# Optimization experiments

Measured on AMD Instinct MI355X. Metric: run time of the kernel, lower is better.

Reference implementation:

```python
import jax, jax.numpy as jnp
import numpy as np

B, N, C, H = 8, 1024, 1024, 16
HD = C // H
SCALE = HD ** -0.5


def setup_inputs() -> dict:
    key = jax.random.key(0)
    ks = jax.random.split(key, 6)
    s = 0.02
    return {
        "x": jax.random.normal(ks[0], (B, N, C), dtype=jnp.float32),
        "z_cls": jax.random.normal(ks[1], (B, 2 * C), dtype=jnp.float32),
        "Wqkv": jax.random.normal(ks[2], (C, 3 * C), dtype=jnp.float32) * s,
        "Wkv_cls": jax.random.normal(ks[3], (2 * C, 2 * C), dtype=jnp.float32) * s,
        "Wproj": jax.random.normal(ks[4], (C, C), dtype=jnp.float32) * s,
        "bproj": jax.random.normal(ks[5], (C,), dtype=jnp.float32) * s,
    }


def reference(x, z_cls, Wqkv, Wkv_cls, Wproj, bproj):
    # qkv projection: [B,N,3C] -> q,k,v each [B,H,N,HD]
    qkv = (x @ Wqkv).reshape(B, N, 3, H, HD).transpose(2, 0, 3, 1, 4)
    q, k, v = qkv[0], qkv[1], qkv[2]
    # cls k/v: [B,2C] -> [B,H,1,HD] each
    kv_cls = (z_cls @ Wkv_cls).reshape(B, 1, 2, H, HD).transpose(2, 0, 3, 1, 4)
    k_cls, v_cls = kv_cls[0], kv_cls[1]
    k = jnp.concatenate([k_cls, k], axis=2)  # [B,H,N+1,HD]
    v = jnp.concatenate([v_cls, v], axis=2)
    attn = jax.nn.softmax(jnp.einsum("bhnd,bhmd->bhnm", q, k) * SCALE, axis=-1)
    out = jnp.einsum("bhnm,bhmd->bhnd", attn, v)  # [B,H,N,HD]
    out = out.transpose(0, 2, 1, 3).reshape(B, N, C)
    return out @ Wproj + bproj
```

## Files before the change

### kernel.cpp

```cpp
#include <hip/hip_runtime.h>


typedef __attribute__((ext_vector_type(8))) short bf16x8;
typedef __attribute__((ext_vector_type(8))) unsigned short u16x8;
typedef __attribute__((ext_vector_type(4))) float f32x4;

#define SL2E 0.18033688011112042f

__device__ __forceinline__ unsigned short f2bf(float f) {
  unsigned int u = __builtin_bit_cast(unsigned int, f);
  return (unsigned short)((u + 0x7FFFu + ((u >> 16) & 1u)) >> 16);
}

__device__ __forceinline__ unsigned int cvt_pk_bf16(float lo, float hi) {
  unsigned int r;
  asm("v_cvt_pk_bf16_f32 %0, %1, %2" : "=v"(r) : "v"(lo), "v"(hi));
  return r;
}

template <typename T>
__device__ __forceinline__ void gll16(const T* g, void* l) {
  __builtin_amdgcn_global_load_lds(
      (__attribute__((address_space(1))) void*)(const_cast<T*>(g)),
      (__attribute__((address_space(3))) void*)l, 16, 0, 0);
}

__global__ __launch_bounds__(256) void cvt_f2b(const float* __restrict__ in,
                                               unsigned short* __restrict__ out, int n) {
  int i = (blockIdx.x * 256 + threadIdx.x) * 8;
  if (i >= n) return;
  const float4* p4 = (const float4*)(in + i);
  float4 a = p4[0], b = p4[1];
  u16x8 o;
  o[0] = f2bf(a.x); o[1] = f2bf(a.y); o[2] = f2bf(a.z); o[3] = f2bf(a.w);
  o[4] = f2bf(b.x); o[5] = f2bf(b.y); o[6] = f2bf(b.z); o[7] = f2bf(b.w);
  *(u16x8*)(out + i) = o;
}

__global__ __launch_bounds__(256) void transpose_f2b(const float* __restrict__ in,
                                                     unsigned short* __restrict__ out,
                                                     int R, int C) {
  __shared__ float tile[32][33];
  int c0 = blockIdx.x * 32, r0 = blockIdx.y * 32;
  int tx = threadIdx.x, ty = threadIdx.y;
#pragma unroll
  for (int j = 0; j < 32; j += 8)
    tile[ty + j][tx] = in[(size_t)(r0 + ty + j) * C + c0 + tx];
  __syncthreads();
#pragma unroll
  for (int j = 0; j < 32; j += 8)
    out[(size_t)(c0 + ty + j) * R + r0 + tx] = f2bf(tile[tx][ty + j]);
}

__global__ __launch_bounds__(256) void kvcls_gemm(const float* __restrict__ z,
                                                  const float* __restrict__ W,
                                                  float* __restrict__ accum) {
  int cc = blockIdx.x >> 5;
  int kc = blockIdx.x & 31;
  int c = cc * 256 + threadIdx.x;
  int k0 = kc * 64;
  float acc[8] = {0, 0, 0, 0, 0, 0, 0, 0};
  const float* wp = W + (size_t)k0 * 2048 + c;
  for (int k = 0; k < 64; ++k) {
    float wv = wp[(size_t)k * 2048];
#pragma unroll
    for (int b = 0; b < 8; ++b) acc[b] += z[b * 2048 + k0 + k] * wv;
  }
#pragma unroll
  for (int b = 0; b < 8; ++b) atomicAdd(&accum[b * 2048 + c], acc[b]);
}

__global__ __launch_bounds__(256) void kvcls_scatter(const float* __restrict__ accum,
                                                     unsigned short* __restrict__ kbuf,
                                                     unsigned short* __restrict__ vbuf) {
  int i = blockIdx.x * 256 + threadIdx.x;
  int b = i >> 11, c = i & 2047;
  int t = c >> 10, h = (c >> 6) & 15, d = c & 63;
  int bh = b * 16 + h;
  unsigned short v = f2bf(accum[i]);
  if (t == 0) kbuf[((size_t)bh * 1088 + 0) * 64 + d] = v;
  else        vbuf[((size_t)bh * 64 + d) * 1088 + 0] = v;
}

__global__ __launch_bounds__(512, 2) void gemm_qkv(const unsigned short* __restrict__ A,
                                                   const unsigned short* __restrict__ Bt,
                                                   unsigned short* __restrict__ qb,
                                                   unsigned short* __restrict__ kbuf,
                                                   unsigned short* __restrict__ vbuf) {
  __shared__ __attribute__((aligned(16))) unsigned short As[2][256 * 64];
  __shared__ __attribute__((aligned(16))) unsigned short Bs[2][256 * 64];
  int t = threadIdx.x, w = t >> 6, l = t & 63;
  int g = l >> 4, q = l & 15;
  int wg = ((int)blockIdx.x & 7) * 48 + ((int)blockIdx.x >> 3);
  int tm = wg / 12, tn = wg % 12;
  int m0 = tm * 256, n0 = tn * 256;
  int wr = w >> 2, wc = w & 3;

  auto STAGE = [&](int bb, int k0) {
#pragma unroll
    for (int i = 0; i < 4; ++i) {
      int f = i * 8192 + t * 16;
      int row = f >> 7, colb = (f & 127) ^ ((row & 7) << 4);
      gll16(A + (size_t)(m0 + row) * 1024 + k0 + (colb >> 1), (char*)As[bb] + f);
    }
#pragma unroll
    for (int i = 0; i < 4; ++i) {
      int f = i * 8192 + t * 16;
      int row = f >> 7, colb = (f & 127) ^ ((row & 7) << 4);
      gll16(Bt + (size_t)(n0 + row) * 1024 + k0 + (colb >> 1), (char*)Bs[bb] + f);
    }
  };

  f32x4 acc[8][4] = {};
  STAGE(0, 0);
  for (int kt = 0; kt < 16; ++kt) {
    int cur = kt & 1;
    if (kt < 15) {
      STAGE(cur ^ 1, (kt + 1) * 64);
      asm volatile("s_waitcnt vmcnt(8)" ::: "memory");
    } else {
      asm volatile("s_waitcnt vmcnt(0)" ::: "memory");
    }
    __builtin_amdgcn_s_barrier();
    asm volatile("" ::: "memory");
    const char* Ac = (const char*)As[cur];
    const char* Bc = (const char*)Bs[cur];
#pragma unroll
    for (int kk = 0; kk < 2; ++kk) {
      bf16x8 af[8], bf[4];
#pragma unroll
      for (int m = 0; m < 8; ++m) {
        int row = wr * 128 + m * 16 + q;
        af[m] = *(const bf16x8*)(Ac + row * 128 + ((kk * 64 + g * 16) ^ ((row & 7) << 4)));
      }
#pragma unroll
      for (int n = 0; n < 4; ++n) {
        int row = wc * 64 + n * 16 + q;
        bf[n] = *(const bf16x8*)(Bc + row * 128 + ((kk * 64 + g * 16) ^ ((row & 7) << 4)));
      }
      __builtin_amdgcn_s_setprio(1);
#pragma unroll
      for (int m = 0; m < 8; ++m)
#pragma unroll
        for (int n = 0; n < 4; ++n)
          acc[m][n] = __builtin_amdgcn_mfma_f32_16x16x32_bf16(af[m], bf[n], acc[m][n], 0, 0, 0);
      __builtin_amdgcn_s_setprio(0);
    }
    asm volatile("" ::: "memory");
    __builtin_amdgcn_s_barrier();
    asm volatile("" ::: "memory");
  }
  int tsel = n0 >> 10;
  int b = m0 >> 10;
  int nqb = m0 & 1023, ncb = n0 & 1023;
#pragma unroll
  for (int m = 0; m < 8; ++m)
#pragma unroll
    for (int n = 0; n < 4; ++n)
#pragma unroll
      for (int r = 0; r < 4; ++r) {
        int nq = nqb + wr * 128 + m * 16 + g * 4 + r;
        int col = ncb + wc * 64 + n * 16 + q;
        int h = col >> 6, d = col & 63;
        int bh = b * 16 + h;
        unsigned short val = f2bf(acc[m][n][r]);
        if (tsel == 0)      qb[((size_t)bh * 1024 + nq) * 64 + d] = val;
        else if (tsel == 1) kbuf[((size_t)bh * 1088 + 1 + nq) * 64 + d] = val;
        else                vbuf[((size_t)bh * 64 + d) * 1088 + 1 + nq] = val;
      }
}

__global__ __launch_bounds__(256) void attn_kernel(const unsigned short* __restrict__ qbuf,
                                                   const unsigned short* __restrict__ kbuf,
                                                   const unsigned short* __restrict__ vbuf,
                                                   unsigned short* __restrict__ ob) {
  __shared__ __attribute__((aligned(16))) unsigned short Ks[2][64 * 64];
  __shared__ __attribute__((aligned(16))) unsigned short Vs[2][64 * 64];
  __shared__ __attribute__((aligned(16))) unsigned short Ps[4][16 * 64];
  int t = threadIdx.x, w = t >> 6, l = t & 63;
  int g = l >> 4, q = l & 15;
  int wg = (blockIdx.x & 7) * 256 + (blockIdx.x >> 3);
  int bh = wg >> 4, qt = wg & 15;

  const unsigned short* qrow = qbuf + ((size_t)bh * 1024 + qt * 64 + w * 16 + q) * 64;
  bf16x8 qf[2];
  qf[0] = *(const bf16x8*)(qrow + g * 8);
  qf[1] = *(const bf16x8*)(qrow + 32 + g * 8);

  const unsigned short* kg = kbuf + (size_t)bh * 1088 * 64;
  const unsigned short* vg = vbuf + (size_t)bh * 64 * 1088;
  char* Pw = (char*)Ps[w];

  auto STAGE = [&](int bb, int kt) {
#pragma unroll
    for (int i = 0; i < 2; ++i) {
      int f = i * 4096 + t * 16;
      int row = f >> 7, colb = (f & 127) ^ ((row & 7) << 4);
      gll16(kg + (size_t)(kt * 64 + row) * 64 + (colb >> 1), (char*)Ks[bb] + f);
      gll16(vg + (size_t)row * 1088 + kt * 64 + (colb >> 1), (char*)Vs[bb] + f);
    }
  };

  STAGE(0, 0);
  __syncthreads();

  f32x4 o[4] = {};
  float mrun = -__builtin_inff(), lrun = 0.f;
  int swz = (q & 7) << 4;

  for (int kt = 0; kt < 17; ++kt) {
    int cur = kt & 1;
    if (kt < 16) STAGE(cur ^ 1, kt + 1);
    f32x4 s[4] = {};
#pragma unroll
    for (int kk = 0; kk < 2; ++kk) {
      bf16x8 kf[4];
#pragma unroll
      for (int n = 0; n < 4; ++n) {
        int cb = (kk * 64 + g * 16) ^ swz;
        kf[n] = *(const bf16x8*)((const char*)Ks[cur] + (n * 16 + q) * 128 + cb);
      }
      __builtin_amdgcn_s_setprio(1);
#pragma unroll
      for (int n = 0; n < 4; ++n)
        s[n] = __builtin_amdgcn_mfma_f32_16x16x32_bf16(kf[n], qf[kk], s[n], 0, 0, 0);
      __builtin_amdgcn_s_setprio(0);
    }
    if (kt == 16) {
#pragma unroll
      for (int n = 0; n < 4; ++n)
#pragma unroll
        for (int r = 0; r < 4; ++r)
          if (n | r) s[n][r] = -__builtin_inff();
      if (g != 0) s[0][0] = -__builtin_inff();
    }
    float mx = fmaxf(fmaxf(fmaxf(s[0][0], s[0][1]), fmaxf(s[0][2], s[0][3])),
                     fmaxf(fmaxf(s[1][0], s[1][1]), fmaxf(s[1][2], s[1][3])));
    mx = fmaxf(mx, fmaxf(fmaxf(fmaxf(s[2][0], s[2][1]), fmaxf(s[2][2], s[2][3])),
                         fmaxf(fmaxf(s[3][0], s[3][1]), fmaxf(s[3][2], s[3][3]))));
    mx = fmaxf(mx, __shfl_xor(mx, 16));
    mx = fmaxf(mx, __shfl_xor(mx, 32));
    float mnew;
    if (__all(mx <= mrun + 64.f)) {
      mnew = mrun;
    } else {
      mnew = fmaxf(mrun, mx);
      float fc = exp2f((mrun - mnew) * SL2E);
      mrun = mnew;
      lrun *= fc;
#pragma unroll
      for (int n = 0; n < 4; ++n) {
        o[n][0] *= fc; o[n][1] *= fc; o[n][2] *= fc; o[n][3] *= fc;
      }
    }
    float nb = mnew * SL2E;
    float rs = 0.f;
#pragma unroll
    for (int n = 0; n < 4; ++n)
#pragma unroll
      for (int r = 0; r < 4; ++r) {
        float p = exp2f(s[n][r] * SL2E - nb);
        s[n][r] = p;
        rs += p;
      }
    rs += __shfl_xor(rs, 16);
    rs += __shfl_xor(rs, 32);
    lrun += rs;
#pragma unroll
    for (int n = 0; n < 4; ++n) {
      uint2 pk;
      pk.x = cvt_pk_bf16(s[n][0], s[n][1]);
      pk.y = cvt_pk_bf16(s[n][2], s[n][3]);
      *(uint2*)(Pw + q * 128 + ((n * 32 + g * 8) ^ swz)) = pk;
    }
    asm volatile("s_waitcnt lgkmcnt(0)" ::: "memory");
#pragma unroll
    for (int kk = 0; kk < 2; ++kk) {
      bf16x8 pb = *(const bf16x8*)(Pw + q * 128 + ((kk * 64 + g * 16) ^ swz));
      bf16x8 vf[4];
#pragma unroll
      for (int n = 0; n < 4; ++n) {
        int cb = (kk * 64 + g * 16) ^ swz;
        vf[n] = *(const bf16x8*)((const char*)Vs[cur] + (n * 16 + q) * 128 + cb);
      }
      __builtin_amdgcn_s_setprio(1);
#pragma unroll
      for (int n = 0; n < 4; ++n)
        o[n] = __builtin_amdgcn_mfma_f32_16x16x32_bf16(vf[n], pb, o[n], 0, 0, 0);
      __builtin_amdgcn_s_setprio(0);
    }
    __syncthreads();
  }
  int b = bh >> 4, h = bh & 15;
  float inv = 1.0f / lrun;
  size_t rowg = (size_t)b * 1024 + qt * 64 + w * 16 + q;
#pragma unroll
  for (int n = 0; n < 4; ++n) {
    uint2 pk;
    pk.x = cvt_pk_bf16(o[n][0] * inv, o[n][1] * inv);
    pk.y = cvt_pk_bf16(o[n][2] * inv, o[n][3] * inv);
    *(uint2*)(ob + rowg * 1024 + h * 64 + n * 16 + g * 4) = pk;
  }
}

__global__ __launch_bounds__(512, 2) void gemm_proj(const unsigned short* __restrict__ A,
                                                    const unsigned short* __restrict__ Bt,
                                                    const float* __restrict__ bias,
                                                    float* __restrict__ out) {
  __shared__ __attribute__((aligned(16))) unsigned short As[2][256 * 64];
  __shared__ __attribute__((aligned(16))) unsigned short Bs[2][128 * 64];
  int t = threadIdx.x, w = t >> 6, l = t & 63;
  int g = l >> 4, q = l & 15;
  int wg = ((int)blockIdx.x & 7) * 32 + ((int)blockIdx.x >> 3);
  int tm = wg / 8, tn = wg % 8;
  int m0 = tm * 256, n0 = tn * 128;
  int wr = w >> 2, wc = w & 3;

  auto STAGE = [&](int bb, int k0) {
#pragma unroll
    for (int i = 0; i < 4; ++i) {
      int f = i * 8192 + t * 16;
      int row = f >> 7, colb = (f & 127) ^ ((row & 7) << 4);
      gll16(A + (size_t)(m0 + row) * 1024 + k0 + (colb >> 1), (char*)As[bb] + f);
    }
#pragma unroll
    for (int i = 0; i < 2; ++i) {
      int f = i * 8192 + t * 16;
      int row = f >> 7, colb = (f & 127) ^ ((row & 7) << 4);
      gll16(Bt + (size_t)(n0 + row) * 1024 + k0 + (colb >> 1), (char*)Bs[bb] + f);
    }
  };

  f32x4 acc[8][2] = {};
  STAGE(0, 0);
  for (int kt = 0; kt < 16; ++kt) {
    int cur = kt & 1;
    if (kt < 15) {
      STAGE(cur ^ 1, (kt + 1) * 64);
      asm volatile("s_waitcnt vmcnt(6)" ::: "memory");
    } else {
      asm volatile("s_waitcnt vmcnt(0)" ::: "memory");
    }
    __builtin_amdgcn_s_barrier();
    asm volatile("" ::: "memory");
    const char* Ac = (const char*)As[cur];
    const char* Bc = (const char*)Bs[cur];
#pragma unroll
    for (int kk = 0; kk < 2; ++kk) {
      bf16x8 af[8], bf[2];
#pragma unroll
      for (int m = 0; m < 8; ++m) {
        int row = wr * 128 + m * 16 + q;
        af[m] = *(const bf16x8*)(Ac + row * 128 + ((kk * 64 + g * 16) ^ ((row & 7) << 4)));
      }
#pragma unroll
      for (int n = 0; n < 2; ++n) {
        int row = wc * 32 + n * 16 + q;
        bf[n] = *(const bf16x8*)(Bc + row * 128 + ((kk * 64 + g * 16) ^ ((row & 7) << 4)));
      }
      __builtin_amdgcn_s_setprio(1);
#pragma unroll
      for (int m = 0; m < 8; ++m)
#pragma unroll
        for (int n = 0; n < 2; ++n)
          acc[m][n] = __builtin_amdgcn_mfma_f32_16x16x32_bf16(af[m], bf[n], acc[m][n], 0, 0, 0);
      __builtin_amdgcn_s_setprio(0);
    }
    asm volatile("" ::: "memory");
    __builtin_amdgcn_s_barrier();
    asm volatile("" ::: "memory");
  }
  float bv[2];
#pragma unroll
  for (int n = 0; n < 2; ++n) bv[n] = bias[n0 + wc * 32 + n * 16 + q];
#pragma unroll
  for (int m = 0; m < 8; ++m)
#pragma unroll
    for (int r = 0; r < 4; ++r) {
      size_t row = m0 + wr * 128 + m * 16 + g * 4 + r;
#pragma unroll
      for (int n = 0; n < 2; ++n) {
        int col = n0 + wc * 32 + n * 16 + q;
        out[row * 1024 + col] = acc[m][n][r] + bv[n];
      }
    }
}

extern "C" void kernel_launch(void* const* d_in, const int* in_sizes, int n_in,
                              void* d_out, int out_size, void* d_ws, size_t ws_size,
                              hipStream_t stream) {
  const float* x       = (const float*)d_in[0];
  const float* z_cls   = (const float*)d_in[1];
  const float* Wqkv    = (const float*)d_in[2];
  const float* Wkv_cls = (const float*)d_in[3];
  const float* Wproj   = (const float*)d_in[4];
  const float* bproj   = (const float*)d_in[5];
  float* out = (float*)d_out;

  char* p = (char*)d_ws;
  unsigned short* x_bf    = (unsigned short*)p; p += (size_t)8192 * 1024 * 2;
  unsigned short* wqkv_t  = (unsigned short*)p; p += (size_t)3072 * 1024 * 2;
  unsigned short* wproj_t = (unsigned short*)p; p += (size_t)1024 * 1024 * 2;
  unsigned short* q_buf   = (unsigned short*)p; p += (size_t)128 * 1024 * 64 * 2;
  unsigned short* k_buf   = (unsigned short*)p; p += (size_t)128 * 1088 * 64 * 2;
  unsigned short* v_buf   = (unsigned short*)p; p += (size_t)128 * 64 * 1088 * 2;
  unsigned short* attn_o  = (unsigned short*)p; p += (size_t)8192 * 1024 * 2;
  float* accum            = (float*)p;          p += (size_t)8 * 2048 * 4;

  hipMemsetAsync(accum, 0, 8 * 2048 * 4, stream);
  cvt_f2b<<<4096, 256, 0, stream>>>(x, x_bf, 8388608);
  transpose_f2b<<<dim3(96, 32), dim3(32, 8), 0, stream>>>(Wqkv, wqkv_t, 1024, 3072);
  transpose_f2b<<<dim3(32, 32), dim3(32, 8), 0, stream>>>(Wproj, wproj_t, 1024, 1024);
  kvcls_gemm<<<256, 256, 0, stream>>>(z_cls, Wkv_cls, accum);
  kvcls_scatter<<<64, 256, 0, stream>>>(accum, k_buf, v_buf);
  gemm_qkv<<<384, 512, 0, stream>>>(x_bf, wqkv_t, q_buf, k_buf, v_buf);
  attn_kernel<<<2048, 256, 0, stream>>>(q_buf, k_buf, v_buf, attn_o);
  gemm_proj<<<256, 512, 0, stream>>>(attn_o, wproj_t, bproj, out);
}
```

Before: 332.2 us.

## Triple-buffer GEMM LDS staging and shrink QKV tile to 256x128

Both GEMMs move from double to triple-buffered LDS staging, prefetching two k-tiles ahead, and split each k-step into two half-M compute phases with an extra barrier. The QKV GEMM tile shrinks from 256x256 to 256x128, doubling its grid to 768 blocks and halving accumulator registers. Launch bounds drop to one block per CU. The aim is to hide global load latency and balance work across CUs. The cost is fewer resident waves and extra barriers.

After: 332.4 us. About the same (+0.1%).

```diff
diff --git a/kernel.cpp b/kernel.cpp
--- a/kernel.cpp
+++ b/kernel.cpp
@@ -82,18 +82,18 @@
   else        vbuf[((size_t)bh * 64 + d) * 1088 + 0] = v;
 }
 
-__global__ __launch_bounds__(512, 2) void gemm_qkv(const unsigned short* __restrict__ A,
+__global__ __launch_bounds__(512, 1) void gemm_qkv(const unsigned short* __restrict__ A,
                                                    const unsigned short* __restrict__ Bt,
                                                    unsigned short* __restrict__ qb,
                                                    unsigned short* __restrict__ kbuf,
                                                    unsigned short* __restrict__ vbuf) {
-  __shared__ __attribute__((aligned(16))) unsigned short As[2][256 * 64];
-  __shared__ __attribute__((aligned(16))) unsigned short Bs[2][256 * 64];
+  __shared__ __attribute__((aligned(16))) unsigned short As[3][256 * 64];
+  __shared__ __attribute__((aligned(16))) unsigned short Bs[3][128 * 64];
   int t = threadIdx.x, w = t >> 6, l = t & 63;
   int g = l >> 4, q = l & 15;
-  int wg = ((int)blockIdx.x & 7) * 48 + ((int)blockIdx.x >> 3);
-  int tm = wg / 12, tn = wg % 12;
-  int m0 = tm * 256, n0 = tn * 256;
+  int wg = ((int)blockIdx.x & 7) * 96 + ((int)blockIdx.x >> 3);
+  int tm = wg / 24, tn = wg % 24;
+  int m0 = tm * 256, n0 = tn * 128;
   int wr = w >> 2, wc = w & 3;
 
   auto STAGE = [&](int bb, int k0) {
@@ -104,51 +104,84 @@
       gll16(A + (size_t)(m0 + row) * 1024 + k0 + (colb >> 1), (char*)As[bb] + f);
     }
 #pragma unroll
-    for (int i = 0; i < 4; ++i) {
+    for (int i = 0; i < 2; ++i) {
       int f = i * 8192 + t * 16;
       int row = f >> 7, colb = (f & 127) ^ ((row & 7) << 4);
       gll16(Bt + (size_t)(n0 + row) * 1024 + k0 + (colb >> 1), (char*)Bs[bb] + f);
     }
   };
 
-  f32x4 acc[8][4] = {};
+  f32x4 acc[8][2] = {};
   STAGE(0, 0);
+  STAGE(1, 64);
+  int bc = 0;
   for (int kt = 0; kt < 16; ++kt) {
-    int cur = kt & 1;
-    if (kt < 15) {
-      STAGE(cur ^ 1, (kt + 1) * 64);
-      asm volatile("s_waitcnt vmcnt(8)" ::: "memory");
+    int bs = bc + 2; if (bs >= 3) bs -= 3;
+    if (kt < 14) {
+      STAGE(bs, (kt + 2) * 64);
+      asm volatile("s_waitcnt vmcnt(12)" ::: "memory");
+    } else if (kt == 14) {
+      asm volatile("s_waitcnt vmcnt(6)" ::: "memory");
     } else {
       asm volatile("s_waitcnt vmcnt(0)" ::: "memory");
     }
     __builtin_amdgcn_s_barrier();
     asm volatile("" ::: "memory");
-    const char* Ac = (const char*)As[cur];
-    const char* Bc = (const char*)Bs[cur];
-#pragma unroll
-    for (int kk = 0; kk < 2; ++kk) {
-      bf16x8 af[8], bf[4];
-#pragma unroll
-      for (int m = 0; m < 8; ++m) {
-        int row = wr * 128 + m * 16 + q;
-        af[m] = *(const bf16x8*)(Ac + row * 128 + ((kk * 64 + g * 16) ^ ((row & 7) << 4)));
-      }
-#pragma unroll
-      for (int n = 0; n < 4; ++n) {
-        int row = wc * 64 + n * 16 + q;
-        bf[n] = *(const bf16x8*)(Bc + row * 128 + ((kk * 64 + g * 16) ^ ((row & 7) << 4)));
-      }
-      __builtin_amdgcn_s_setprio(1);
-#pragma unroll
-      for (int m = 0; m < 8; ++m)
-#pragma unroll
-        for (int n = 0; n < 4; ++n)
-          acc[m][n] = __builtin_amdgcn_mfma_f32_16x16x32_bf16(af[m], bf[n], acc[m][n], 0, 0, 0);
-      __builtin_amdgcn_s_setprio(0);
-    }
-    asm volatile("" ::: "memory");
-    __builtin_amdgcn_s_barrier();
-    asm volatile("" ::: "memory");
+    const char* Ac = (const char*)As[bc];
+    const char* Bc = (const char*)Bs[bc];
+    bf16x8 bfr[2][2];
+#pragma unroll
+    for (int n = 0; n < 2; ++n)
+#pragma unroll
+      for (int kk = 0; kk < 2; ++kk) {
+        int row = wc * 32 + n * 16 + q;
+        bfr[n][kk] = *(const bf16x8*)(Bc + row * 128 + ((kk * 64 + g * 16) ^ ((row & 7) << 4)));
+      }
+    {
+      bf16x8 afr[4][2];
+#pragma unroll
+      for (int m = 0; m < 4; ++m)
+#pragma unroll
+        for (int kk = 0; kk < 2; ++kk) {
+          int row = wr * 128 + m * 16 + q;
+          afr[m][kk] = *(const bf16x8*)(Ac + row * 128 + ((kk * 64 + g * 16) ^ ((row & 7) << 4)));
+        }
+      __builtin_amdgcn_s_setprio(1);
+#pragma unroll
+      for (int m = 0; m < 4; ++m)
+#pragma unroll
+        for (int n = 0; n < 2; ++n)
+#pragma unroll
+          for (int kk = 0; kk < 2; ++kk)
+            acc[m][n] = __builtin_amdgcn_mfma_f32_16x16x32_bf16(afr[m][kk], bfr[n][kk], acc[m][n], 0, 0, 0);
+      __builtin_amdgcn_s_setprio(0);
+    }
+    asm volatile("" ::: "memory");
+    __builtin_amdgcn_s_barrier();
+    asm volatile("" ::: "memory");
+    {
+      bf16x8 afr[4][2];
+#pragma unroll
+      for (int m = 0; m < 4; ++m)
+#pragma unroll
+        for (int kk = 0; kk < 2; ++kk) {
+          int row = wr * 128 + (m + 4) * 16 + q;
+          afr[m][kk] = *(const bf16x8*)(Ac + row * 128 + ((kk * 64 + g * 16) ^ ((row & 7) << 4)));
+        }
+      __builtin_amdgcn_s_setprio(1);
+#pragma unroll
+      for (int m = 0; m < 4; ++m)
+#pragma unroll
+        for (int n = 0; n < 2; ++n)
+#pragma unroll
+          for (int kk = 0; kk < 2; ++kk)
+            acc[m + 4][n] = __builtin_amdgcn_mfma_f32_16x16x32_bf16(afr[m][kk], bfr[n][kk], acc[m + 4][n], 0, 0, 0);
+      __builtin_amdgcn_s_setprio(0);
+    }
+    asm volatile("" ::: "memory");
+    __builtin_amdgcn_s_barrier();
+    asm volatile("" ::: "memory");
+    bc = bc + 1; if (bc >= 3) bc = 0;
   }
   int tsel = n0 >> 10;
   int b = m0 >> 10;
@@ -156,11 +189,11 @@
 #pragma unroll
   for (int m = 0; m < 8; ++m)
 #pragma unroll
-    for (int n = 0; n < 4; ++n)
+    for (int n = 0; n < 2; ++n)
 #pragma unroll
       for (int r = 0; r < 4; ++r) {
         int nq = nqb + wr * 128 + m * 16 + g * 4 + r;
-        int col = ncb + wc * 64 + n * 16 + q;
+        int col = ncb + wc * 32 + n * 16 + q;
         int h = col >> 6, d = col & 63;
         int bh = b * 16 + h;
         unsigned short val = f2bf(acc[m][n][r]);
@@ -303,12 +336,12 @@
   }
 }
 
-__global__ __launch_bounds__(512, 2) void gemm_proj(const unsigned short* __restrict__ A,
+__global__ __launch_bounds__(512, 1) void gemm_proj(const unsigned short* __restrict__ A,
                                                     const unsigned short* __restrict__ Bt,
                                                     const float* __restrict__ bias,
                                                     float* __restrict__ out) {
-  __shared__ __attribute__((aligned(16))) unsigned short As[2][256 * 64];
-  __shared__ __attribute__((aligned(16))) unsigned short Bs[2][128 * 64];
+  __shared__ __attribute__((aligned(16))) unsigned short As[3][256 * 64];
+  __shared__ __attribute__((aligned(16))) unsigned short Bs[3][128 * 64];
   int t = threadIdx.x, w = t >> 6, l = t & 63;
   int g = l >> 4, q = l & 15;
   int wg = ((int)blockIdx.x & 7) * 32 + ((int)blockIdx.x >> 3);
@@ -333,42 +366,75 @@
 
   f32x4 acc[8][2] = {};
   STAGE(0, 0);
+  STAGE(1, 64);
+  int bc = 0;
   for (int kt = 0; kt < 16; ++kt) {
-    int cur = kt & 1;
-    if (kt < 15) {
-      STAGE(cur ^ 1, (kt + 1) * 64);
+    int bs = bc + 2; if (bs >= 3) bs -= 3;
+    if (kt < 14) {
+      STAGE(bs, (kt + 2) * 64);
+      asm volatile("s_waitcnt vmcnt(12)" ::: "memory");
+    } else if (kt == 14) {
       asm volatile("s_waitcnt vmcnt(6)" ::: "memory");
     } else {
       asm volatile("s_waitcnt vmcnt(0)" ::: "memory");
     }
     __builtin_amdgcn_s_barrier();
     asm volatile("" ::: "memory");
-    const char* Ac = (const char*)As[cur];
-    const char* Bc = (const char*)Bs[cur];
-#pragma unroll
-    for (int kk = 0; kk < 2; ++kk) {
-      bf16x8 af[8], bf[2];
-#pragma unroll
-      for (int m = 0; m < 8; ++m) {
-        int row = wr * 128 + m * 16 + q;
-        af[m] = *(const bf16x8*)(Ac + row * 128 + ((kk * 64 + g * 16) ^ ((row & 7) << 4)));
-      }
-#pragma unroll
-      for (int n = 0; n < 2; ++n) {
+    const char* Ac = (const char*)As[bc];
+    const char* Bc = (const char*)Bs[bc];
+    bf16x8 bfr[2][2];
+#pragma unroll
+    for (int n = 0; n < 2; ++n)
+#pragma unroll
+      for (int kk = 0; kk < 2; ++kk) {
         int row = wc * 32 + n * 16 + q;
-        bf[n] = *(const bf16x8*)(Bc + row * 128 + ((kk * 64 + g * 16) ^ ((row & 7) << 4)));
-      }
-      __builtin_amdgcn_s_setprio(1);
-#pragma unroll
-      for (int m = 0; m < 8; ++m)
+        bfr[n][kk] = *(const bf16x8*)(Bc + row * 128 + ((kk * 64 + g * 16) ^ ((row & 7) << 4)));
+      }
+    {
+      bf16x8 afr[4][2];
+#pragma unroll
+      for (int m = 0; m < 4; ++m)
+#pragma unroll
+        for (int kk = 0; kk < 2; ++kk) {
+          int row = wr * 128 + m * 16 + q;
+          afr[m][kk] = *(const bf16x8*)(Ac + row * 128 + ((kk * 64 + g * 16) ^ ((row & 7) << 4)));
+        }
+      __builtin_amdgcn_s_setprio(1);
+#pragma unroll
+      for (int m = 0; m < 4; ++m)
 #pragma unroll
         for (int n = 0; n < 2; ++n)
-          acc[m][n] = __builtin_amdgcn_mfma_f32_16x16x32_bf16(af[m], bf[n], acc[m][n], 0, 0, 0);
-      __builtin_amdgcn_s_setprio(0);
-    }
-    asm volatile("" ::: "memory");
-    __builtin_amdgcn_s_barrier();
-    asm volatile("" ::: "memory");
+#pragma unroll
+          for (int kk = 0; kk < 2; ++kk)
+            acc[m][n] = __builtin_amdgcn_mfma_f32_16x16x32_bf16(afr[m][kk], bfr[n][kk], acc[m][n], 0, 0, 0);
+      __builtin_amdgcn_s_setprio(0);
+    }
+    asm volatile("" ::: "memory");
+    __builtin_amdgcn_s_barrier();
+    asm volatile("" ::: "memory");
+    {
+      bf16x8 afr[4][2];
+#pragma unroll
+      for (int m = 0; m < 4; ++m)
+#pragma unroll
+        for (int kk = 0; kk < 2; ++kk) {
+          int row = wr * 128 + (m + 4) * 16 + q;
+          afr[m][kk] = *(const bf16x8*)(Ac + row * 128 + ((kk * 64 + g * 16) ^ ((row & 7) << 4)));
+        }
+      __builtin_amdgcn_s_setprio(1);
+#pragma unroll
+      for (int m = 0; m < 4; ++m)
+#pragma unroll
+        for (int n = 0; n < 2; ++n)
+#pragma unroll
+          for (int kk = 0; kk < 2; ++kk)
+            acc[m + 4][n] = __builtin_amdgcn_mfma_f32_16x16x32_bf16(afr[m][kk], bfr[n][kk], acc[m + 4][n], 0, 0, 0);
+      __builtin_amdgcn_s_setprio(0);
+    }
+    asm volatile("" ::: "memory");
+    __builtin_amdgcn_s_barrier();
+    asm volatile("" ::: "memory");
+    bc = bc + 1; if (bc >= 3) bc = 0;
   }
   float bv[2];
 #pragma unroll
@@ -413,7 +479,7 @@
   transpose_f2b<<<dim3(32, 32), dim3(32, 8), 0, stream>>>(Wproj, wproj_t, 1024, 1024);
   kvcls_gemm<<<256, 256, 0, stream>>>(z_cls, Wkv_cls, accum);
   kvcls_scatter<<<64, 256, 0, stream>>>(accum, k_buf, v_buf);
-  gemm_qkv<<<384, 512, 0, stream>>>(x_bf, wqkv_t, q_buf, k_buf, v_buf);
+  gemm_qkv<<<768, 512, 0, stream>>>(x_bf, wqkv_t, q_buf, k_buf, v_buf);
   attn_kernel<<<2048, 256, 0, stream>>>(q_buf, k_buf, v_buf, attn_o);
   gemm_proj<<<256, 512, 0, stream>>>(attn_o, wproj_t, bproj, out);
 }
```
